# Optimization experiments

Hardware: AMD Instinct MI355X
Metric: run time of the kernel (lower is better)

## Reference

```python
import jax, jax.numpy as jnp
import numpy as np

E = 2048      # n_embd
H = 16        # n_head
D = E // H    # head_dim = 128
QR = 64       # q_lora_rank
KR = D        # kv_lora_rank = 128
RD = 64       # rotary_dim
EPS = 1e-5
ROPE_BASE = 10000.0


def _layernorm(x, w):
    mu = jnp.mean(x, axis=-1, keepdims=True)
    var = jnp.mean(jnp.square(x - mu), axis=-1, keepdims=True)
    return (x - mu) * jax.lax.rsqrt(var + EPS) * w


def _apply_rope(x, cos, sin):
    # x: [b, s, h, d]; rotate first RD dims, pass the rest through
    xr, xp = x[..., :RD], x[..., RD:]
    half = RD // 2
    rot = jnp.concatenate([-xr[..., half:], xr[..., :half]], axis=-1)
    return jnp.concatenate([xr * cos + rot * sin, xp], axis=-1)


def setup_inputs() -> dict:
    key = jax.random.key(0)
    ks = jax.random.split(key, 8)
    s = 0.02
    return {
        "x": jax.random.normal(ks[0], (2, 2048, E), dtype=jnp.float32),
        "g_q": jnp.ones((E,), dtype=jnp.float32),
        "g_kv": jnp.ones((E,), dtype=jnp.float32),
        "w_qa": jax.random.normal(ks[1], (E, QR), dtype=jnp.float32) * s,
        "w_qb": jax.random.normal(ks[2], (QR, E), dtype=jnp.float32) * s,
        "w_kva": jax.random.normal(ks[3], (E, KR + H * 2 * D), dtype=jnp.float32) * s,
        "w_kvb": jax.random.normal(ks[4], (KR, E), dtype=jnp.float32) * s,
        "w_o": jax.random.normal(ks[5], (E, E), dtype=jnp.float32) * s,
    }


def reference(x, g_q, g_kv, w_qa, w_qb, w_kva, w_kvb, w_o):
    b, s, _ = x.shape
    # low-rank Q: LN -> down (QR) -> up (E)
    q = (_layernorm(x, g_q) @ w_qa) @ w_qb          # [b, s, E]
    q = q.reshape(b, s, H, D)
    # KV path: LN -> joint proj [KR + H*2*D]
    kv = _layernorm(x, g_kv) @ w_kva                # [b, s, KR + 4096]
    kc, vv = kv[..., :KR], kv[..., KR:]
    k = (kc @ w_kvb).reshape(b, s, H, D)            # decompress K
    v = vv.reshape(b, s, H, 2, D)[..., 0, :]        # take first of the 2 stacked slices
    # RoPE on first RD dims
    inv_freq = 1.0 / (ROPE_BASE ** (jnp.arange(0, RD, 2, dtype=jnp.float32) / RD))
    freqs = jnp.arange(s, dtype=jnp.float32)[:, None] * inv_freq[None, :]  # [s, RD/2]
    emb = jnp.concatenate([freqs, freqs], axis=-1)                         # [s, RD]
    cos = jnp.cos(emb)[None, :, None, :]
    sin = jnp.sin(emb)[None, :, None, :]
    q = _apply_rope(q, cos, sin)
    k = _apply_rope(k, cos, sin)
    # causal SDPA
    att = jnp.einsum("bqhd,bkhd->bhqk", q, k) * (1.0 / jnp.sqrt(jnp.float32(D)))
    causal = jnp.tril(jnp.ones((s, s), dtype=bool))
    att = jnp.where(causal, att, jnp.finfo(att.dtype).min)
    att = jax.nn.softmax(att, axis=-1)
    y = jnp.einsum("bhqk,bkhd->bqhd", att, v).reshape(b, s, E)
    return y @ w_o
```

## Files before the change

### kernel.cpp

```cpp
#include <hip/hip_runtime.h>
#include <cstdint>
#include <cstddef>

typedef unsigned short u16;
typedef __attribute__((ext_vector_type(8))) __bf16 bf16x8;
typedef __attribute__((ext_vector_type(4))) float f32x4;
typedef __attribute__((ext_vector_type(16))) float f32x16;
typedef __attribute__((ext_vector_type(4))) unsigned u32x4;

#define E_ 2048
#define H_ 16
#define D_ 128
#define QR_ 64
#define KR_ 128
#define S_ 2048
#define B_ 2
#define T_ 4096
#define NSEL_ 2176
#define EPS_ 1e-5f
#define SCALE_ 0.08838834764831845f
#define SCL2_ 0.12751743f

typedef __attribute__((address_space(1))) const void gvoid;
typedef __attribute__((address_space(3))) void lvoid;

__device__ __forceinline__ u16 f2bf(float f) {
  unsigned u = __float_as_uint(f);
  unsigned r = (u + 0x7FFFu + ((u >> 16) & 1u)) >> 16;
  return (u16)r;
}

__global__ __launch_bounds__(256) void k_ln(
    const float* __restrict__ x, const float* __restrict__ gq,
    const float* __restrict__ gkv, u16* __restrict__ lnq, u16* __restrict__ lnkv,
    float* __restrict__ cos_t, float* __restrict__ sin_t) {
  if (blockIdx.x < (S_ * 32) / 256) {
    int idx = blockIdx.x * 256 + threadIdx.x;
    int t = idx >> 5, j = idx & 31;
    float inv = powf(10000.0f, -(float)j / 32.0f);
    float a = (float)t * inv;
    cos_t[idx] = cosf(a);
    sin_t[idx] = sinf(a);
  }
  int row = blockIdx.x;
  const float* xr = x + (size_t)row * E_;
  int base = threadIdx.x * 8;
  float4 v0 = *(const float4*)(xr + base);
  float4 v1 = *(const float4*)(xr + base + 4);
  float xv[8] = {v0.x, v0.y, v0.z, v0.w, v1.x, v1.y, v1.z, v1.w};
  float s0 = 0.f, s1 = 0.f;
#pragma unroll
  for (int i = 0; i < 8; i++) { s0 += xv[i]; s1 += xv[i] * xv[i]; }
  for (int off = 32; off > 0; off >>= 1) {
    s0 += __shfl_down(s0, off);
    s1 += __shfl_down(s1, off);
  }
  __shared__ float red[2][4];
  int wid = threadIdx.x >> 6, lane = threadIdx.x & 63;
  if (lane == 0) { red[0][wid] = s0; red[1][wid] = s1; }
  __syncthreads();
  s0 = red[0][0] + red[0][1] + red[0][2] + red[0][3];
  s1 = red[1][0] + red[1][1] + red[1][2] + red[1][3];
  float mu = s0 * (1.0f / E_);
  float var = s1 * (1.0f / E_) - mu * mu;
  float rs = rsqrtf(var + EPS_);
  u16 oq[8], okv[8];
#pragma unroll
  for (int i = 0; i < 8; i++) {
    float nv = (xv[i] - mu) * rs;
    oq[i] = f2bf(nv * gq[base + i]);
    okv[i] = f2bf(nv * gkv[base + i]);
  }
  *(ushort4*)(lnq + (size_t)row * E_ + base) = make_ushort4(oq[0], oq[1], oq[2], oq[3]);
  *(ushort4*)(lnq + (size_t)row * E_ + base + 4) = make_ushort4(oq[4], oq[5], oq[6], oq[7]);
  *(ushort4*)(lnkv + (size_t)row * E_ + base) = make_ushort4(okv[0], okv[1], okv[2], okv[3]);
  *(ushort4*)(lnkv + (size_t)row * E_ + base + 4) = make_ushort4(okv[4], okv[5], okv[6], okv[7]);
}

__global__ __launch_bounds__(256) void k_transp_all(
    const float* __restrict__ w_qa, const float* __restrict__ w_qb,
    const float* __restrict__ w_kvb, const float* __restrict__ w_o,
    const float* __restrict__ w_kva,
    u16* __restrict__ wqa_t, u16* __restrict__ wqb_t, u16* __restrict__ wkvb_t,
    u16* __restrict__ wo_t, u16* __restrict__ wsel_t) {
  __shared__ float t[32][33];
  int f = blockIdx.x;
  const float* in;
  u16* out;
  int K, Nin, bx, by;
  bool sel = false;
  if (f < 128) {
    in = w_qb; out = wqb_t; K = QR_; Nin = E_; bx = f % 64; by = f / 64;
  } else if (f < 256) {
    f -= 128;
    in = w_qa; out = wqa_t; K = E_; Nin = QR_; bx = f % 2; by = f / 2;
  } else if (f < 512) {
    f -= 256;
    in = w_kvb; out = wkvb_t; K = KR_; Nin = E_; bx = f % 64; by = f / 64;
  } else if (f < 4608) {
    f -= 512;
    in = w_o; out = wo_t; K = E_; Nin = E_; bx = f % 64; by = f / 64;
  } else {
    f -= 4608;
    in = w_kva; out = wsel_t; K = E_; Nin = 128 + H_ * 2 * D_; sel = true;
    bx = f % 68; by = f / 68;
  }
  int orb = bx * 32;
  int icb;
  if (sel) {
    icb = (orb < 128) ? orb : 128 + ((orb - 128) >> 7) * 256 + ((orb - 128) & 127);
  } else {
    icb = orb;
  }
  int kb = by * 32;
  int r = threadIdx.x >> 3, q = threadIdx.x & 7;
  float4 lv = *(const float4*)&in[(size_t)(kb + r) * Nin + icb + q * 4];
  t[r][q * 4 + 0] = lv.x;
  t[r][q * 4 + 1] = lv.y;
  t[r][q * 4 + 2] = lv.z;
  t[r][q * 4 + 3] = lv.w;
  __syncthreads();
  int c = r;
  ushort4 sv;
  sv.x = f2bf(t[q * 4 + 0][c]);
  sv.y = f2bf(t[q * 4 + 1][c]);
  sv.z = f2bf(t[q * 4 + 2][c]);
  sv.w = f2bf(t[q * 4 + 3][c]);
  *(ushort4*)&out[(size_t)(orb + c) * K + kb + q * 4] = sv;
}

__global__ __launch_bounds__(256) void k_vtr(
    const u16* __restrict__ vn, u16* __restrict__ vt) {
  __shared__ u16 t[64][68];
  int c0 = blockIdx.x * 64;
  int b = blockIdx.y >> 5;
  int s0 = (blockIdx.y & 31) * 64;
#pragma unroll
  for (int i = 0; i < 4; i++) {
    int flat = threadIdx.x + i * 256;
    int r = flat >> 4, q = flat & 15;
    ushort4 v = *(const ushort4*)&vn[((size_t)(b * 2048 + s0 + r)) * 2048 + c0 + q * 4];
    t[r][q * 4 + 0] = v.x;
    t[r][q * 4 + 1] = v.y;
    t[r][q * 4 + 2] = v.z;
    t[r][q * 4 + 3] = v.w;
  }
  __syncthreads();
#pragma unroll
  for (int i = 0; i < 4; i++) {
    int flat = threadIdx.x + i * 256;
    int c = flat >> 4, q = flat & 15;
    ushort4 v;
    v.x = t[q * 4 + 0][c];
    v.y = t[q * 4 + 1][c];
    v.z = t[q * 4 + 2][c];
    v.w = t[q * 4 + 3][c];
    *(ushort4*)&vt[((size_t)(b * 2048 + c0 + c)) * 2048 + s0 + q * 4] = v;
  }
}

struct EpiP {
  float* of32;
  u16* obf;
  u16* kc;
  u16* vt;
  u16* qk;
  const float* cost;
  const float* sint;
};

template <int BM, int BN, int EPI>
__global__ __launch_bounds__(256, 3) void k_gemm(
    const u16* __restrict__ A, const u16* __restrict__ Bt,
    int M, int N, int K, EpiP ep) {
  constexpr int WM = BM / 2;
  constexpr int MI = WM / 16;
  constexpr int WN = BN / 2;
  constexpr int NI = WN / 16;
  __shared__ alignas(16) u16 lsA[2][BM * 32];
  __shared__ alignas(16) u16 lsB[2][BN * 32];
  int tid = threadIdx.x, lane = tid & 63, wid = tid >> 6;
  int wr = wid >> 1, wc = wid & 1;
  int gx = gridDim.x;
  int nwg = gx * gridDim.y;
  int flat = blockIdx.y * gx + blockIdx.x;
  int cpx = nwg >> 3;
  int swz = (flat & 7) * cpx + (flat >> 3);
  int bm = swz / gx, bn = swz % gx;
  f32x4 zero4 = {0.f, 0.f, 0.f, 0.f};
  f32x4 acc[MI][NI];
#pragma unroll
  for (int m = 0; m < MI; m++)
#pragma unroll
    for (int n = 0; n < NI; n++) acc[m][n] = zero4;
  const int nkt = K >> 5;
  const u16* Ab = A + (size_t)bm * BM * K;
  const u16* Bb = Bt + (size_t)bn * BN * K;
  int arow = tid >> 2, acol8 = (tid & 3) * 8;
  int lg = lane >> 4, li = lane & 15;

  auto stage = [&](int buf, int kt) {
    int k0 = kt * 32;
#pragma unroll
    for (int c = 0; c < BM / 64; c++) {
      int row = c * 64 + arow;
      __builtin_amdgcn_global_load_lds(
          (gvoid*)(Ab + (size_t)row * K + k0 + acol8),
          (lvoid*)(&lsA[buf][row * 32 + acol8]), 16, 0, 0);
    }
#pragma unroll
    for (int c = 0; c < BN / 64; c++) {
      int row = c * 64 + arow;
      __builtin_amdgcn_global_load_lds(
          (gvoid*)(Bb + (size_t)row * K + k0 + acol8),
          (lvoid*)(&lsB[buf][row * 32 + acol8]), 16, 0, 0);
    }
  };

  stage(0, 0);
  asm volatile("s_waitcnt vmcnt(0)" ::: "memory");
  __builtin_amdgcn_s_barrier();
  asm volatile("" ::: "memory");
  for (int kt = 0; kt < nkt; ++kt) {
    int cur = kt & 1;
    if (kt + 1 < nkt) stage(cur ^ 1, kt + 1);
    bf16x8 af[MI], bfr[NI];
#pragma unroll
    for (int m = 0; m < MI; m++)
      af[m] = *reinterpret_cast<const bf16x8*>(&lsA[cur][(wr * WM + m * 16 + li) * 32 + lg * 8]);
#pragma unroll
    for (int n = 0; n < NI; n++)
      bfr[n] = *reinterpret_cast<const bf16x8*>(&lsB[cur][(wc * WN + n * 16 + li) * 32 + lg * 8]);
#pragma unroll
    for (int m = 0; m < MI; m++)
#pragma unroll
      for (int n = 0; n < NI; n++)
        acc[m][n] = __builtin_amdgcn_mfma_f32_16x16x32_bf16(af[m], bfr[n], acc[m][n], 0, 0, 0);
    asm volatile("s_waitcnt vmcnt(0)" ::: "memory");
    __builtin_amdgcn_s_barrier();
    asm volatile("" ::: "memory");
  }
#pragma unroll
  for (int m = 0; m < MI; m++) {
#pragma unroll
    for (int n = 0; n < NI; n++) {
      int col = bn * BN + wc * WN + n * 16 + li;
#pragma unroll
      for (int r = 0; r < 4; r++) {
        int row = bm * BM + wr * WM + m * 16 + lg * 4 + r;
        float val = acc[m][n][r];
        if constexpr (EPI == 0) {
          ep.obf[(size_t)row * 64 + col] = f2bf(val);
        } else if constexpr (EPI == 1) {
          ep.of32[(size_t)row * E_ + col] = val;
        } else if constexpr (EPI == 2) {
          if (col < KR_) {
            ep.kc[(size_t)row * KR_ + col] = f2bf(val);
          } else {
            ep.vt[(size_t)row * 2048 + (col - KR_)] = f2bf(val);
          }
        } else {
          int h = col >> 7, dl = col & 127;
          int b = row >> 11, sp = row & 2047;
          float outv;
          if (dl < 64) {
            float pv = acc[m][n ^ 2][r];
            int j = dl & 31;
            float c = ep.cost[sp * 32 + j];
            float s = ep.sint[sp * 32 + j];
            float rot = (dl < 32) ? -pv : pv;
            outv = val * c + rot * s;
          } else {
            outv = val;
          }
          ep.qk[((size_t)(b * H_ + h) * S_ + sp) * D_ + dl] = f2bf(outv);
        }
      }
    }
  }
}

__global__ __launch_bounds__(256, 2) void k_attn(
    const u16* __restrict__ q_r, const u16* __restrict__ k_r,
    const u16* __restrict__ v_t, u16* __restrict__ y) {
  __shared__ alignas(16) u16 Ks[2][2][32 * 128];
  __shared__ alignas(16) u16 Vs[2][2][64 * 64];
  __shared__ float Ml[2][2][32];
  int tid = threadIdx.x, lane = tid & 63, wid = tid >> 6;
  int id = blockIdx.x;
  int bh = ((id & 7) << 2) | ((id >> 3) & 3);
  int j = 31 - (id >> 5);
  int w2 = wid & 1, grp = wid >> 1;
  int b = bh >> 4, h = bh & 15;
  int li = lane & 31, hi = lane >> 5;
  int qb = 64 * j + w2 * 32;
  int qrow = qb + li;
  int n = j + 1;
  int kg_base = grp * 32 * n;
  const u16* qbase = q_r + (size_t)bh * S_ * D_;
  const u16* kbase = k_r + (size_t)bh * S_ * D_;
  const u16* vbase = v_t + (size_t)bh * D_ * S_;

  bf16x8 aq[8];
#pragma unroll
  for (int step = 0; step < 8; step++)
    aq[step] = *(const bf16x8*)&qbase[(size_t)qrow * D_ + step * 16 + hi * 8];

  f32x16 o[4];
#pragma unroll
  for (int dt = 0; dt < 4; dt++)
#pragma unroll
    for (int r = 0; r < 16; r++) o[dt][r] = 0.f;
  float mreg = -1e30f, lreg = 0.f;

  int kr_l = w2 * 16 + (lane >> 4);
  int kc_l = (lane & 15) * 8;
  int kswz = (li & 7) << 4;

  auto stage = [&](int nb, int p) {
    int kg0 = kg_base + p * 32;
    u16* Kst = &Ks[nb][grp][0];
    u16* Vst = &Vs[nb][grp][0];
#pragma unroll
    for (int i = 0; i < 4; i++) {
      int r = kr_l + i * 4;
      __builtin_amdgcn_global_load_lds(
          (gvoid*)(kbase + (size_t)(kg0 + r) * D_ + (kc_l ^ ((r & 7) << 3))),
          (lvoid*)(&Kst[r * 128 + kc_l]), 16, 0, 0);
    }
#pragma unroll
    for (int i = 0; i < 4; i++) {
      int r = w2 * 32 + i * 8 + (lane >> 3);
      int ss = lane & 7;
      int s = ss ^ (r & 7);
      int d = ((s >> 2) << 6) + r;
      int kk = kg0 + (s & 3) * 8;
      __builtin_amdgcn_global_load_lds(
          (gvoid*)(vbase + (size_t)d * S_ + kk),
          (lvoid*)(&Vst[r * 64 + ss * 8]), 16, 0, 0);
    }
  };

  stage(0, 0);
  int cbuf = 0;

  for (int p = 0; p < n; ++p) {
    int kg0 = kg_base + p * 32;
    asm volatile("s_waitcnt vmcnt(0)" ::: "memory");
    __builtin_amdgcn_s_barrier();
    asm volatile("" ::: "memory");
    if (p + 1 < n) stage(cbuf ^ 1, p + 1);
    if (kg0 <= qb + 31) {
      bool domask = (kg0 + 31 > qb);
      const char* Kc = (const char*)&Ks[cbuf][grp][0];
      const char* Vc = (const char*)&Vs[cbuf][grp][0];
      bf16x8 kf[8];
#pragma unroll
      for (int step = 0; step < 8; step++)
        kf[step] = *(const bf16x8*)(Kc + li * 256 + ((step * 32 + hi * 16) ^ kswz));
      f32x16 c0, c1;
#pragma unroll
      for (int r = 0; r < 16; r++) { c0[r] = 0.f; c1[r] = 0.f; }
      __builtin_amdgcn_s_setprio(1);
#pragma unroll
      for (int step = 0; step < 4; step++) {
        c0 = __builtin_amdgcn_mfma_f32_32x32x16_bf16(kf[step], aq[step], c0, 0, 0, 0);
        c1 = __builtin_amdgcn_mfma_f32_32x32x16_bf16(kf[step + 4], aq[step + 4], c1, 0, 0, 0);
      }
      __builtin_amdgcn_s_setprio(0);
      float ps[16];
#pragma unroll
      for (int r = 0; r < 16; r++) ps[r] = (c0[r] + c1[r]) * SCL2_;
      if (domask) {
#pragma unroll
        for (int r = 0; r < 16; r++) {
          int k = kg0 + (r & 3) + 8 * (r >> 2) + 4 * hi;
          if (k > qrow) ps[r] = -1e30f;
        }
      }
      float t8[8];
#pragma unroll
      for (int r = 0; r < 8; r++) t8[r] = fmaxf(ps[r], ps[r + 8]);
#pragma unroll
      for (int r = 0; r < 4; r++) t8[r] = fmaxf(t8[r], t8[r + 4]);
      float mt = fmaxf(fmaxf(t8[0], t8[1]), fmaxf(t8[2], t8[3]));
      mt = fmaxf(mt, __shfl_xor(mt, 32));
      if (!__all(mt <= mreg + 8.f)) {
        float mn = fmaxf(mreg, mt);
        float al = __builtin_amdgcn_exp2f(mreg - mn);
        mreg = mn;
        lreg *= al;
#pragma unroll
        for (int dt = 0; dt < 4; dt++)
#pragma unroll
          for (int r = 0; r < 16; r++) o[dt][r] *= al;
      }
#pragma unroll
      for (int r = 0; r < 16; r++) ps[r] = __builtin_amdgcn_exp2f(ps[r] - mreg);
      float s8[8];
#pragma unroll
      for (int r = 0; r < 8; r++) s8[r] = ps[r] + ps[r + 8];
#pragma unroll
      for (int r = 0; r < 4; r++) s8[r] = s8[r] + s8[r + 4];
      float rs = (s8[0] + s8[1]) + (s8[2] + s8[3]);
      rs += __shfl_xor(rs, 32);
      lreg += rs;
#pragma unroll
      for (int ks = 0; ks < 2; ks++) {
        const int bix = ks * 8;
        unsigned P0, P1, P2, P3;
        asm("v_cvt_pk_bf16_f32 %0, %1, %2" : "=v"(P0) : "v"(ps[bix + 0]), "v"(ps[bix + 1]));
        asm("v_cvt_pk_bf16_f32 %0, %1, %2" : "=v"(P1) : "v"(ps[bix + 2]), "v"(ps[bix + 3]));
        asm("v_cvt_pk_bf16_f32 %0, %1, %2" : "=v"(P2) : "v"(ps[bix + 4]), "v"(ps[bix + 5]));
        asm("v_cvt_pk_bf16_f32 %0, %1, %2" : "=v"(P3) : "v"(ps[bix + 6]), "v"(ps[bix + 7]));
        asm("v_permlane32_swap_b32 %0, %1" : "+v"(P0), "+v"(P2));
        asm("v_permlane32_swap_b32 %0, %1" : "+v"(P1), "+v"(P3));
        bf16x8 bp = __builtin_bit_cast(bf16x8, (u32x4){P0, P1, P2, P3});
        bf16x8 vf[4];
#pragma unroll
        for (int dt = 0; dt < 4; dt++) {
          int row = ((dt & 1) << 5) + li;
          vf[dt] = *(const bf16x8*)(Vc + row * 128 +
                                    ((((dt >> 1) * 4 + ks * 2 + hi) * 16) ^ ((row & 7) << 4)));
        }
        __builtin_amdgcn_s_setprio(1);
#pragma unroll
        for (int dt = 0; dt < 4; dt++)
          o[dt] = __builtin_amdgcn_mfma_f32_32x32x16_bf16(vf[dt], bp, o[dt], 0, 0, 0);
        __builtin_amdgcn_s_setprio(0);
      }
    }
    cbuf ^= 1;
  }
  __syncthreads();
  float* fb = (float*)&Ks[0][0][0] + w2 * 4096;
  if (grp == 0) {
#pragma unroll
    for (int k = 0; k < 64; ++k) fb[k * 64 + lane] = o[k >> 4][k & 15];
    if (lane < 32) {
      Ml[w2][0][li] = mreg;
      Ml[w2][1][li] = lreg;
    }
  }
  __syncthreads();
  if (grp == 1) {
    float m1 = Ml[w2][0][li], l1 = Ml[w2][1][li];
    float m = fmaxf(mreg, m1);
    float s2 = __builtin_amdgcn_exp2f(mreg - m);
    float s1 = __builtin_amdgcn_exp2f(m1 - m);
    float lsum = lreg * s2 + l1 * s1;
    float rl = 1.0f / lsum;
    u16* yrow = y + ((size_t)(b * S_ + qrow)) * E_ + h * D_;
#pragma unroll
    for (int dt = 0; dt < 4; dt++) {
#pragma unroll
      for (int g2 = 0; g2 < 4; g2++) {
        int d = dt * 32 + 8 * g2 + 4 * hi;
        ushort4 sv;
        float v0 = (o[dt][4 * g2 + 0] * s2 + fb[(dt * 16 + 4 * g2 + 0) * 64 + lane] * s1) * rl;
        float v1 = (o[dt][4 * g2 + 1] * s2 + fb[(dt * 16 + 4 * g2 + 1) * 64 + lane] * s1) * rl;
        float v2 = (o[dt][4 * g2 + 2] * s2 + fb[(dt * 16 + 4 * g2 + 2) * 64 + lane] * s1) * rl;
        float v3 = (o[dt][4 * g2 + 3] * s2 + fb[(dt * 16 + 4 * g2 + 3) * 64 + lane] * s1) * rl;
        sv.x = f2bf(v0);
        sv.y = f2bf(v1);
        sv.z = f2bf(v2);
        sv.w = f2bf(v3);
        *(ushort4*)(yrow + d) = sv;
      }
    }
  }
}

extern "C" void kernel_launch(void* const* d_in, const int* in_sizes, int n_in,
                              void* d_out, int out_size, void* d_ws, size_t ws_size,
                              hipStream_t stream) {
  const float* x = (const float*)d_in[0];
  const float* g_q = (const float*)d_in[1];
  const float* g_kv = (const float*)d_in[2];
  const float* w_qa = (const float*)d_in[3];
  const float* w_qb = (const float*)d_in[4];
  const float* w_kva = (const float*)d_in[5];
  const float* w_kvb = (const float*)d_in[6];
  const float* w_o = (const float*)d_in[7];
  float* out = (float*)d_out;
  char* ws = (char*)d_ws;

  size_t off = 0;
  float* cos_t = (float*)(ws + off); off += (size_t)S_ * 32 * 4;
  float* sin_t = (float*)(ws + off); off += (size_t)S_ * 32 * 4;
  u16* wqa_t = (u16*)(ws + off); off += (size_t)QR_ * E_ * 2;
  u16* wqb_t = (u16*)(ws + off); off += (size_t)E_ * QR_ * 2;
  u16* wkvb_t = (u16*)(ws + off); off += (size_t)E_ * KR_ * 2;
  u16* wo_t = (u16*)(ws + off); off += (size_t)E_ * E_ * 2;
  u16* wsel_t = (u16*)(ws + off); off += (size_t)NSEL_ * E_ * 2;
  u16* qlow = (u16*)(ws + off); off += (size_t)T_ * QR_ * 2;
  u16* kc = (u16*)(ws + off); off += (size_t)T_ * KR_ * 2;
  u16* ln_q = (u16*)(ws + off); off += (size_t)T_ * E_ * 2;
  u16* ln_kv = (u16*)(ws + off); off += (size_t)T_ * E_ * 2;
  u16* k_rb = (u16*)(ws + off); off += (size_t)T_ * E_ * 2;
  u16* v_tb = (u16*)(ws + off); off += (size_t)T_ * E_ * 2;
  u16* y = ln_q;
  u16* q_rb = ln_kv;
  u16* v_nat = k_rb;

  k_ln<<<dim3(T_), dim3(256), 0, stream>>>(x, g_q, g_kv, ln_q, ln_kv, cos_t, sin_t);

  k_transp_all<<<dim3(8960), dim3(256), 0, stream>>>(
      w_qa, w_qb, w_kvb, w_o, w_kva, wqa_t, wqb_t, wkvb_t, wo_t, wsel_t);

  EpiP ep{};

  ep = EpiP{}; ep.obf = qlow;
  k_gemm<64, 64, 0><<<dim3(1, T_ / 64), dim3(256), 0, stream>>>(ln_q, wqa_t, T_, QR_, E_, ep);

  ep = EpiP{}; ep.kc = kc; ep.vt = v_nat;
  k_gemm<128, 128, 2><<<dim3(NSEL_ / 128, T_ / 128), dim3(256), 0, stream>>>(ln_kv, wsel_t, T_, NSEL_, E_, ep);

  ep = EpiP{}; ep.qk = q_rb; ep.cost = cos_t; ep.sint = sin_t;
  k_gemm<128, 128, 3><<<dim3(E_ / 128, T_ / 128), dim3(256), 0, stream>>>(qlow, wqb_t, T_, E_, QR_, ep);

  k_vtr<<<dim3(32, 64), dim3(256), 0, stream>>>(v_nat, v_tb);

  ep = EpiP{}; ep.qk = k_rb; ep.cost = cos_t; ep.sint = sin_t;
  k_gemm<128, 128, 3><<<dim3(E_ / 128, T_ / 128), dim3(256), 0, stream>>>(kc, wkvb_t, T_, E_, KR_, ep);

  k_attn<<<dim3(1024), dim3(256), 0, stream>>>(q_rb, k_rb, v_tb, y);

  ep = EpiP{}; ep.of32 = out;
  k_gemm<128, 128, 1><<<dim3(E_ / 128, T_ / 128), dim3(256), 0, stream>>>(y, wo_t, T_, E_, E_, ep);
}
```

Baseline: 249.1 us.

## Merge independent GEMM launches into combined grids for QA/KV and Q/K rope

The Q down-projection GEMM and the joint KV projection GEMM now run as one launch, with block index ranges routed to each body. The Q-up and K-decompress rope GEMMs are likewise merged into one 1024-block launch. This removes two kernel launches and lets small, under-occupying GEMMs fill the GPU alongside larger ones. The shared-memory buffer is sized for the largest tile, which may affect occupancy for the small-tile path. An unused label is left in the host code.

```diff
diff --git a/kernel.cpp b/kernel.cpp
--- a/kernel.cpp
+++ b/kernel.cpp
@@ -170,23 +170,17 @@
 };
 
 template <int BM, int BN, int EPI>
-__global__ __launch_bounds__(256, 3) void k_gemm(
+__device__ __forceinline__ void gemm_body(
     const u16* __restrict__ A, const u16* __restrict__ Bt,
-    int M, int N, int K, EpiP ep) {
+    int K, EpiP ep, int bm, int bn, u16* ls) {
   constexpr int WM = BM / 2;
   constexpr int MI = WM / 16;
   constexpr int WN = BN / 2;
   constexpr int NI = WN / 16;
-  __shared__ alignas(16) u16 lsA[2][BM * 32];
-  __shared__ alignas(16) u16 lsB[2][BN * 32];
+  u16* lsA = ls;
+  u16* lsB = ls + 2 * BM * 32;
   int tid = threadIdx.x, lane = tid & 63, wid = tid >> 6;
   int wr = wid >> 1, wc = wid & 1;
-  int gx = gridDim.x;
-  int nwg = gx * gridDim.y;
-  int flat = blockIdx.y * gx + blockIdx.x;
-  int cpx = nwg >> 3;
-  int swz = (flat & 7) * cpx + (flat >> 3);
-  int bm = swz / gx, bn = swz % gx;
   f32x4 zero4 = {0.f, 0.f, 0.f, 0.f};
   f32x4 acc[MI][NI];
 #pragma unroll
@@ -206,14 +200,14 @@
       int row = c * 64 + arow;
       __builtin_amdgcn_global_load_lds(
           (gvoid*)(Ab + (size_t)row * K + k0 + acol8),
-          (lvoid*)(&lsA[buf][row * 32 + acol8]), 16, 0, 0);
+          (lvoid*)(&lsA[buf * BM * 32 + row * 32 + acol8]), 16, 0, 0);
     }
 #pragma unroll
     for (int c = 0; c < BN / 64; c++) {
       int row = c * 64 + arow;
       __builtin_amdgcn_global_load_lds(
           (gvoid*)(Bb + (size_t)row * K + k0 + acol8),
-          (lvoid*)(&lsB[buf][row * 32 + acol8]), 16, 0, 0);
+          (lvoid*)(&lsB[buf * BN * 32 + row * 32 + acol8]), 16, 0, 0);
     }
   };
 
@@ -227,10 +221,12 @@
     bf16x8 af[MI], bfr[NI];
 #pragma unroll
     for (int m = 0; m < MI; m++)
-      af[m] = *reinterpret_cast<const bf16x8*>(&lsA[cur][(wr * WM + m * 16 + li) * 32 + lg * 8]);
+      af[m] = *reinterpret_cast<const bf16x8*>(
+          &lsA[cur * BM * 32 + (wr * WM + m * 16 + li) * 32 + lg * 8]);
 #pragma unroll
     for (int n = 0; n < NI; n++)
-      bfr[n] = *reinterpret_cast<const bf16x8*>(&lsB[cur][(wc * WN + n * 16 + li) * 32 + lg * 8]);
+      bfr[n] = *reinterpret_cast<const bf16x8*>(
+          &lsB[cur * BN * 32 + (wc * WN + n * 16 + li) * 32 + lg * 8]);
 #pragma unroll
     for (int m = 0; m < MI; m++)
 #pragma unroll
@@ -280,6 +276,64 @@
   }
 }
 
+template <int BM, int BN, int EPI>
+__global__ __launch_bounds__(256, 3) void k_gemm(
+    const u16* __restrict__ A, const u16* __restrict__ Bt,
+    int M, int N, int K, EpiP ep) {
+  __shared__ alignas(16) u16 ls[2 * BM * 32 + 2 * BN * 32];
+  int gx = gridDim.x;
+  int nwg = gx * gridDim.y;
+  int flat = blockIdx.y * gx + blockIdx.x;
+  int cpx = nwg >> 3;
+  int swz = (flat & 7) * cpx + (flat >> 3);
+  int bm = swz / gx, bn = swz % gx;
+  gemm_body<BM, BN, EPI>(A, Bt, K, ep, bm, bn, ls);
+}
+
+__global__ __launch_bounds__(256, 3) void k_gemm_qakv(
+    const u16* __restrict__ lnq, const u16* __restrict__ wqa, u16* __restrict__ qlow,
+    const u16* __restrict__ lnkv, const u16* __restrict__ wsel,
+    u16* __restrict__ kc, u16* __restrict__ vnat) {
+  __shared__ alignas(16) u16 ls[2 * 128 * 32 + 2 * 128 * 32];
+  int f = blockIdx.x;
+  if (f < 544) {
+    int swz = (f & 7) * 68 + (f >> 3);
+    int bm = swz / 17, bn = swz % 17;
+    EpiP ep{};
+    ep.kc = kc;
+    ep.vt = vnat;
+    gemm_body<128, 128, 2>(lnkv, wsel, E_, ep, bm, bn, ls);
+  } else {
+    int lf = f - 544;
+    int bm = (lf & 7) * 8 + (lf >> 3);
+    EpiP ep{};
+    ep.obf = qlow;
+    gemm_body<64, 64, 0>(lnq, wqa, E_, ep, bm, 0, ls);
+  }
+}
+
+__global__ __launch_bounds__(256, 3) void k_gemm_rope2(
+    const u16* __restrict__ Aq, const u16* __restrict__ Btq, u16* __restrict__ outq,
+    const u16* __restrict__ Ak, const u16* __restrict__ Btk, u16* __restrict__ outk,
+    const float* __restrict__ cost, const float* __restrict__ sint) {
+  __shared__ alignas(16) u16 ls[2 * 128 * 32 + 2 * 128 * 32];
+  int f = blockIdx.x;
+  bool isK = f >= 512;
+  int lf = f & 511;
+  int swz = (lf & 7) * 64 + (lf >> 3);
+  int bm = swz >> 4, bn = swz & 15;
+  EpiP ep{};
+  ep.cost = cost;
+  ep.sint = sint;
+  if (isK) {
+    ep.qk = outk;
+    gemm_body<128, 128, 3>(Ak, Btk, KR_, ep, bm, bn, ls);
+  } else {
+    ep.qk = outq;
+    gemm_body<128, 128, 3>(Aq, Btq, QR_, ep, bm, bn, ls);
+  }
+}
+
 __global__ __launch_bounds__(256, 2) void k_attn(
     const u16* __restrict__ q_r, const u16* __restrict__ k_r,
     const u16* __restrict__ v_t, u16* __restrict__ y) {
@@ -508,24 +562,20 @@
   k_transp_all<<<dim3(8960), dim3(256), 0, stream>>>(
       w_qa, w_qb, w_kvb, w_o, w_kva, wqa_t, wqb_t, wkvb_t, wo_t, wsel_t);
 
-  EpiP ep{};
-
-  ep = EpiP{}; ep.obf = qlow;
-  k_gemm<64, 64, 0><<<dim3(1, T_ / 64), dim3(256), 0, stream>>>(ln_q, wqa_t, T_, QR_, E_, ep);
-
-  ep = EpiP{}; ep.kc = kc; ep.vt = v_nat;
-  k_gemm<128, 128, 2><<<dim3(NSEL_ / 128, T_ / 128), dim3(256), 0, stream>>>(ln_kv, wsel_t, T_, NSEL_, E_, ep);
-
-  ep = EpiP{}; ep.qk = q_rb; ep.cost = cos_t; ep.sint = sin_t;
-  k_gemm<128, 128, 3><<<dim3(E_ / 128, T_ / 128), dim3(256), 0, stream>>>(qlow, wqb_t, T_, E_, QR_, ep);
+  k_gemm_qakv<<<dim3(608), dim3(256), 0, stream>>>(
+      ln_q, wqa_t, qlow, ln_kv, wsel_t, kc, v_nat);
 
   k_vtr<<<dim3(32, 64), dim3(256), 0, stream>>>(v_nat, v_tb);
 
-  ep = EpiP{}; ep.qk = k_rb; ep.cost = cos_t; ep.sint = sin_t;
-  k_gemm<128, 128, 3><<<dim3(E_ / 128, T_ / 128), dim3(256), 0, stream>>>(kc, wkvb_t, T_, E_, KR_, ep);
+  k_gemm_rope2<<<dim3(1024), dim3(256), 0, stream>>>(
+      qlow, wqb_t, q_rb, kc, wkvb_t, k_rb, cos_t, sin_t);
 
   k_attn<<<dim3(1024), dim3(256), 0, stream>>>(q_rb, k_rb, v_tb, y);
 
-  ep = EpiP{}; ep.of32 = out;
-  k_gemm<128, 128, 1><<<dim3(E_ / 128, T_ / 128), dim3(256), 0, stream>>>(y, wo_t, T_, E_, E_, ep);
-}
+  ep_out:
+  {
+    EpiP ep{};
+    ep.of32 = out;
+    k_gemm<128, 128, 1><<<dim3(E_ / 128, T_ / 128), dim3(256), 0, stream>>>(y, wo_t, T_, E_, E_, ep);
+  }
+}
```

After: 203.7 us. -18.2%, faster.
